# Kernel tuning notes

Measured on AMD Instinct MI355X. Metric: run time of the kernel, lower is better.

Reference implementation:

```python
import jax, jax.numpy as jnp
import numpy as np
import math

NUM_V = 32; NUM_K = 16; DK = 128; DV = 128; KCONV = 4; H = 2048
KEY_DIM = NUM_K * DK          # 2048
VALUE_DIM = NUM_V * DV        # 4096
CONV_DIM = 2 * KEY_DIM + VALUE_DIM  # 8192
EPS = 1e-6
VPK = NUM_V // NUM_K


def setup_inputs() -> dict:
    key = jax.random.key(0)
    ks = jax.random.split(key, 12)
    s = 0.02  # weight scale for numerical sanity
    return {
        "hidden_in": jax.random.normal(ks[0], (1, 1, H), jnp.float32),
        "conv_state": jax.random.normal(ks[1], (1, CONV_DIM, KCONV), jnp.float32),
        "rec_state": jax.random.normal(ks[2], (1, NUM_V, DK, DV), jnp.float32) * s,
        "W_qkv": jax.random.normal(ks[3], (CONV_DIM, H), jnp.float32) * s,
        "W_z": jax.random.normal(ks[4], (VALUE_DIM, H), jnp.float32) * s,
        "W_b": jax.random.normal(ks[5], (NUM_V, H), jnp.float32) * s,
        "W_a": jax.random.normal(ks[6], (NUM_V, H), jnp.float32) * s,
        "W_out": jax.random.normal(ks[7], (H, VALUE_DIM), jnp.float32) * s,
        "conv_w": jax.random.normal(ks[8], (CONV_DIM, KCONV), jnp.float32) * s,
        "dt_bias": jax.random.normal(ks[9], (NUM_V,), jnp.float32),
        "A_log": jax.random.normal(ks[10], (NUM_V,), jnp.float32),
        "norm_w": jnp.ones((DV,), jnp.float32),
    }


def _l2norm(x, eps=1e-6):
    return x * jax.lax.rsqrt(jnp.sum(x * x, axis=-1, keepdims=True) + eps)


def reference(hidden_in, conv_state, rec_state, W_qkv, W_z, W_b, W_a,
              W_out, conv_w, dt_bias, A_log, norm_w):
    h = hidden_in[0, 0]                       # (H,)
    mixed = W_qkv @ h                         # (CONV_DIM,)
    z = W_z @ h                               # (VALUE_DIM,)
    b = W_b @ h                               # (NUM_V,)
    a = W_a @ h                               # (NUM_V,)

    # causal conv1d update: shift state by one, take dot with kernel
    w = jnp.concatenate([conv_state, mixed[None, :, None]], axis=-1)  # (1, C, K+1)
    new_conv_state = w[:, :, 1:]                                      # (1, C, K)
    conv_out = jax.nn.silu(jnp.sum(new_conv_state * conv_w[None], axis=-1))[0]  # (C,)

    q = conv_out[:KEY_DIM].reshape(NUM_K, DK)
    k = conv_out[KEY_DIM:2 * KEY_DIM].reshape(NUM_K, DK)
    v = conv_out[2 * KEY_DIM:].reshape(NUM_V, DV)
    q = jnp.repeat(q, VPK, axis=0)            # (NUM_V, DK)
    k = jnp.repeat(k, VPK, axis=0)

    q = _l2norm(q) * (1.0 / math.sqrt(DK))
    k = _l2norm(k)

    beta = jax.nn.sigmoid(b)                                  # (NUM_V,)
    g = -jnp.exp(A_log) * jax.nn.softplus(a + dt_bias)        # (NUM_V,)

    # gated delta-rule recurrent update
    rec = rec_state[0] * jnp.exp(g)[:, None, None]            # (NUM_V, DK, DV)
    kv_mem = jnp.einsum('hkd,hk->hd', rec, k)                 # (NUM_V, DV)
    delta = (v - kv_mem) * beta[:, None]
    rec = rec + k[:, :, None] * delta[:, None, :]
    core = jnp.einsum('hkd,hk->hd', rec, q)                   # (NUM_V, DV)

    # gated RMSNorm over Dv per head
    var = jnp.mean(core * core, axis=-1, keepdims=True)
    xn = core * jax.lax.rsqrt(var + EPS) * norm_w
    zf = z.reshape(NUM_V, DV)
    out = (xn * jax.nn.silu(zf)).reshape(VALUE_DIM)

    hidden_out = (W_out @ out).reshape(1, 1, H)
    return (hidden_out, new_conv_state, rec[None])
```

## Files before the change

### kernel.cpp

```cpp
#include <hip/hip_runtime.h>

#define HDIM 2048
#define NUM_V 32
#define NUM_K 16
#define DK 128
#define DV 128
#define KEY_DIM 2048
#define VALUE_DIM 4096
#define CONV_DIM 8192
#define TOTAL_ROWS 12352



typedef __attribute__((ext_vector_type(4))) float f32x4;

__global__ __launch_bounds__(256) void k1_gemv(
    const float* __restrict__ h,
    const float* __restrict__ Wqkv,
    const float* __restrict__ Wz,
    const float* __restrict__ Wb,
    const float* __restrict__ Wa,
    const float* __restrict__ conv_state,
    const float* __restrict__ conv_w,
    float* __restrict__ ws,
    float* __restrict__ out_conv)
{
    const int row  = (blockIdx.x * 256 + threadIdx.x) >> 6;
    const int lane = threadIdx.x & 63;
    if (row >= TOTAL_ROWS) return;

    const float* wrow;
    if (row < 8192)       wrow = Wqkv + (size_t)row * HDIM;
    else if (row < 12288) wrow = Wz   + (size_t)(row - 8192) * HDIM;
    else if (row < 12320) wrow = Wb   + (size_t)(row - 12288) * HDIM;
    else                  wrow = Wa   + (size_t)(row - 12320) * HDIM;

    float acc = 0.f;
#pragma unroll
    for (int i = 0; i < 8; ++i) {
        const int idx = (i * 64 + lane) * 4;
        f32x4 w4 = *reinterpret_cast<const f32x4*>(wrow + idx);
        f32x4 h4 = *reinterpret_cast<const f32x4*>(h + idx);
        acc += w4.x * h4.x + w4.y * h4.y + w4.z * h4.z + w4.w * h4.w;
    }
#pragma unroll
    for (int off = 32; off > 0; off >>= 1)
        acc += __shfl_down(acc, off, 64);

    if (lane == 0) {
        if (row < 8192) {
            f32x4 cs = *reinterpret_cast<const f32x4*>(conv_state + row * 4);
            f32x4 cw = *reinterpret_cast<const f32x4*>(conv_w + row * 4);
            float pre = cs.y * cw.x + cs.z * cw.y + cs.w * cw.z + acc * cw.w;
            ws[row] = pre / (1.f + expf(-pre));
            f32x4 n; n.x = cs.y; n.y = cs.z; n.z = cs.w; n.w = acc;
            *reinterpret_cast<f32x4*>(out_conv + row * 4) = n;
        } else {
            ws[row] = acc;
        }
    }
}

__global__ __launch_bounds__(1024) void k2_rec(
    const float* __restrict__ ws,
    const float* __restrict__ rec_in,
    const float* __restrict__ dt_bias,
    const float* __restrict__ A_log,
    const float* __restrict__ norm_w,
    float* __restrict__ rec_out,
    float* __restrict__ out_vec)
{
    __shared__ float s_k[128];
    __shared__ float s_q[128];
    __shared__ float s_delta[128];
    __shared__ float s_part[8][128];
    __shared__ float s_red[4];

    const int hh  = blockIdx.x;
    const int t   = threadIdx.x;
    const int d   = t & 127;
    const int kkb = t >> 7;
    const int kh  = hh >> 1;

    const float bv    = ws[12288 + hh];
    const float av    = ws[12320 + hh];
    const float beta  = 1.f / (1.f + expf(-bv));
    const float x     = av + dt_bias[hh];
    const float sp    = fmaxf(x, 0.f) + log1pf(expf(-fabsf(x)));
    const float decay = expf(-expf(A_log[hh]) * sp);

    float qr = 0.f, kr = 0.f;
    if (t < 128) {
        qr = ws[kh * 128 + d];
        kr = ws[KEY_DIM + kh * 128 + d];
        float sq = qr * qr, sk = kr * kr;
#pragma unroll
        for (int off = 32; off > 0; off >>= 1) {
            sq += __shfl_down(sq, off, 64);
            sk += __shfl_down(sk, off, 64);
        }
        if ((t & 63) == 0) { s_red[t >> 6] = sq; s_red[2 + (t >> 6)] = sk; }
    }
    __syncthreads();
    if (t < 128) {
        const float ssq = s_red[0] + s_red[1];
        const float ssk = s_red[2] + s_red[3];
        s_q[d] = qr * rsqrtf(ssq + 1e-6f) * 0.08838834764831845f;
        s_k[d] = kr * rsqrtf(ssk + 1e-6f);
    }
    __syncthreads();

    const float* rrow = rec_in  + (size_t)hh * (DK * DV) + kkb * 16 * DV;
    float*       wrow = rec_out + (size_t)hh * (DK * DV) + kkb * 16 * DV;

    float rv[16];
#pragma unroll
    for (int i = 0; i < 16; ++i)
        rv[i] = rrow[i * DV + d];

    float kvp = 0.f;
#pragma unroll
    for (int i = 0; i < 16; ++i)
        kvp += rv[i] * s_k[kkb * 16 + i];
    s_part[kkb][d] = kvp;
    __syncthreads();

    if (t < 128) {
        float kv = 0.f;
#pragma unroll
        for (int j = 0; j < 8; ++j) kv += s_part[j][d];
        kv *= decay;
        const float vv = ws[2 * KEY_DIM + hh * 128 + d];
        s_delta[d] = (vv - kv) * beta;
    }
    __syncthreads();

    const float dlt = s_delta[d];
    float corep = 0.f;
#pragma unroll
    for (int i = 0; i < 16; ++i) {
        const float r = rv[i] * decay + s_k[kkb * 16 + i] * dlt;
        wrow[i * DV + d] = r;
        corep += r * s_q[kkb * 16 + i];
    }
    s_part[kkb][d] = corep;
    __syncthreads();

    float core = 0.f;
    if (t < 128) {
#pragma unroll
        for (int j = 0; j < 8; ++j) core += s_part[j][d];
        float sc = core * core;
#pragma unroll
        for (int off = 32; off > 0; off >>= 1)
            sc += __shfl_down(sc, off, 64);
        if ((t & 63) == 0) s_red[t >> 6] = sc;
    }
    __syncthreads();
    if (t < 128) {
        const float ssc = s_red[0] + s_red[1];
        const float xn  = core * rsqrtf(ssc * (1.f / 128.f) + 1e-6f) * norm_w[d];
        const float zv  = ws[8192 + hh * 128 + d];
        out_vec[hh * 128 + d] = xn * (zv / (1.f + expf(-zv)));
    }
}

__global__ __launch_bounds__(256) void k3_out(
    const float* __restrict__ Wout,
    const float* __restrict__ out_vec,
    float* __restrict__ hidden_out)
{
    const int row  = (blockIdx.x * 256 + threadIdx.x) >> 6;
    const int lane = threadIdx.x & 63;
    if (row >= HDIM) return;

    const float* wrow = Wout + (size_t)row * VALUE_DIM;
    float acc = 0.f;
#pragma unroll
    for (int i = 0; i < 16; ++i) {
        const int idx = (i * 64 + lane) * 4;
        f32x4 w4 = *reinterpret_cast<const f32x4*>(wrow + idx);
        f32x4 o4 = *reinterpret_cast<const f32x4*>(out_vec + idx);
        acc += w4.x * o4.x + w4.y * o4.y + w4.z * o4.z + w4.w * o4.w;
    }
#pragma unroll
    for (int off = 32; off > 0; off >>= 1)
        acc += __shfl_down(acc, off, 64);
    if (lane == 0) hidden_out[row] = acc;
}

extern "C" void kernel_launch(void* const* d_in, const int* in_sizes, int n_in,
                              void* d_out, int out_size, void* d_ws, size_t ws_size,
                              hipStream_t stream) {
    const float* hidden_in  = (const float*)d_in[0];
    const float* conv_state = (const float*)d_in[1];
    const float* rec_state  = (const float*)d_in[2];
    const float* W_qkv      = (const float*)d_in[3];
    const float* W_z        = (const float*)d_in[4];
    const float* W_b        = (const float*)d_in[5];
    const float* W_a        = (const float*)d_in[6];
    const float* W_out      = (const float*)d_in[7];
    const float* conv_w     = (const float*)d_in[8];
    const float* dt_bias    = (const float*)d_in[9];
    const float* A_log      = (const float*)d_in[10];
    const float* norm_w     = (const float*)d_in[11];

    float* out = (float*)d_out;
    float* ws  = (float*)d_ws;

    k1_gemv<<<TOTAL_ROWS / 4, 256, 0, stream>>>(hidden_in, W_qkv, W_z, W_b, W_a,
                                                conv_state, conv_w, ws, out + 2048);
    k2_rec<<<NUM_V, 1024, 0, stream>>>(ws, rec_state, dt_bias, A_log, norm_w,
                                       out + 2048 + CONV_DIM * 4, ws + 12352);
    k3_out<<<HDIM / 4, 256, 0, stream>>>(W_out, ws + 12352, out);
}
```

Before: 32.12 us.

## Split recurrent kernel across DV slices and move gated RMSNorm into output GEMV

Result: slower. 33.82 us (+5.3%).

```diff
diff --git a/kernel.cpp b/kernel.cpp
--- a/kernel.cpp
+++ b/kernel.cpp
@@ -9,7 +9,6 @@
 #define VALUE_DIM 4096
 #define CONV_DIM 8192
 #define TOTAL_ROWS 12352
-
 
 
 typedef __attribute__((ext_vector_type(4))) float f32x4;
@@ -66,21 +65,24 @@
     const float* __restrict__ rec_in,
     const float* __restrict__ dt_bias,
     const float* __restrict__ A_log,
-    const float* __restrict__ norm_w,
     float* __restrict__ rec_out,
-    float* __restrict__ out_vec)
+    float* __restrict__ core_out)
 {
     __shared__ float s_k[128];
     __shared__ float s_q[128];
-    __shared__ float s_delta[128];
-    __shared__ float s_part[8][128];
+    __shared__ float s_part[16][32];
+    __shared__ float s_delta[32];
     __shared__ float s_red[4];
 
-    const int hh  = blockIdx.x;
-    const int t   = threadIdx.x;
-    const int d   = t & 127;
-    const int kkb = t >> 7;
-    const int kh  = hh >> 1;
+    const int bx   = blockIdx.x;
+    const int hh   = bx >> 2;
+    const int D0   = (bx & 3) * 32;
+    const int t    = threadIdx.x;
+    const int lane = t & 63;
+    const int wid  = t >> 6;
+    const int kkb  = t >> 3;
+    const int dq4  = t & 7;
+    const int kh   = hh >> 1;
 
     const float bv    = ws[12288 + hh];
     const float av    = ws[12320 + hh];
@@ -91,8 +93,8 @@
 
     float qr = 0.f, kr = 0.f;
     if (t < 128) {
-        qr = ws[kh * 128 + d];
-        kr = ws[KEY_DIM + kh * 128 + d];
+        qr = ws[kh * 128 + t];
+        kr = ws[KEY_DIM + kh * 128 + t];
         float sq = qr * qr, sk = kr * kr;
 #pragma unroll
         for (int off = 32; off > 0; off >>= 1) {
@@ -103,84 +105,111 @@
     }
     __syncthreads();
     if (t < 128) {
-        const float ssq = s_red[0] + s_red[1];
-        const float ssk = s_red[2] + s_red[3];
-        s_q[d] = qr * rsqrtf(ssq + 1e-6f) * 0.08838834764831845f;
-        s_k[d] = kr * rsqrtf(ssk + 1e-6f);
-    }
-    __syncthreads();
-
-    const float* rrow = rec_in  + (size_t)hh * (DK * DV) + kkb * 16 * DV;
-    float*       wrow = rec_out + (size_t)hh * (DK * DV) + kkb * 16 * DV;
-
-    float rv[16];
-#pragma unroll
-    for (int i = 0; i < 16; ++i)
-        rv[i] = rrow[i * DV + d];
-
-    float kvp = 0.f;
-#pragma unroll
-    for (int i = 0; i < 16; ++i)
-        kvp += rv[i] * s_k[kkb * 16 + i];
-    s_part[kkb][d] = kvp;
-    __syncthreads();
-
-    if (t < 128) {
+        s_q[t] = qr * rsqrtf(s_red[0] + s_red[1] + 1e-6f) * 0.08838834764831845f;
+        s_k[t] = kr * rsqrtf(s_red[2] + s_red[3] + 1e-6f);
+    }
+    __syncthreads();
+
+    const size_t off0 = (size_t)hh * (DK * DV) + (size_t)kkb * DV + D0 + dq4 * 4;
+    const f32x4 rv = *reinterpret_cast<const f32x4*>(rec_in + off0);
+    const float sk = s_k[kkb];
+    const float sq = s_q[kkb];
+
+    f32x4 kvp = rv * sk;
+#pragma unroll
+    for (int off = 32; off >= 8; off >>= 1) {
+        kvp.x += __shfl_down(kvp.x, off, 64);
+        kvp.y += __shfl_down(kvp.y, off, 64);
+        kvp.z += __shfl_down(kvp.z, off, 64);
+        kvp.w += __shfl_down(kvp.w, off, 64);
+    }
+    if (lane < 8) *reinterpret_cast<f32x4*>(&s_part[wid][lane * 4]) = kvp;
+    __syncthreads();
+
+    if (t < 32) {
         float kv = 0.f;
 #pragma unroll
-        for (int j = 0; j < 8; ++j) kv += s_part[j][d];
+        for (int w = 0; w < 16; ++w) kv += s_part[w][t];
         kv *= decay;
-        const float vv = ws[2 * KEY_DIM + hh * 128 + d];
-        s_delta[d] = (vv - kv) * beta;
-    }
-    __syncthreads();
-
-    const float dlt = s_delta[d];
-    float corep = 0.f;
-#pragma unroll
-    for (int i = 0; i < 16; ++i) {
-        const float r = rv[i] * decay + s_k[kkb * 16 + i] * dlt;
-        wrow[i * DV + d] = r;
-        corep += r * s_q[kkb * 16 + i];
-    }
-    s_part[kkb][d] = corep;
-    __syncthreads();
-
-    float core = 0.f;
-    if (t < 128) {
-#pragma unroll
-        for (int j = 0; j < 8; ++j) core += s_part[j][d];
-        float sc = core * core;
-#pragma unroll
-        for (int off = 32; off > 0; off >>= 1)
-            sc += __shfl_down(sc, off, 64);
-        if ((t & 63) == 0) s_red[t >> 6] = sc;
-    }
-    __syncthreads();
-    if (t < 128) {
-        const float ssc = s_red[0] + s_red[1];
-        const float xn  = core * rsqrtf(ssc * (1.f / 128.f) + 1e-6f) * norm_w[d];
-        const float zv  = ws[8192 + hh * 128 + d];
-        out_vec[hh * 128 + d] = xn * (zv / (1.f + expf(-zv)));
+        const float vv = ws[2 * KEY_DIM + hh * 128 + D0 + t];
+        s_delta[t] = (vv - kv) * beta;
+    }
+    __syncthreads();
+
+    const f32x4 dlt = *reinterpret_cast<const f32x4*>(&s_delta[dq4 * 4]);
+    f32x4 r = rv * decay + dlt * sk;
+    *reinterpret_cast<f32x4*>(rec_out + off0) = r;
+    f32x4 cp = r * sq;
+#pragma unroll
+    for (int off = 32; off >= 8; off >>= 1) {
+        cp.x += __shfl_down(cp.x, off, 64);
+        cp.y += __shfl_down(cp.y, off, 64);
+        cp.z += __shfl_down(cp.z, off, 64);
+        cp.w += __shfl_down(cp.w, off, 64);
+    }
+    if (lane < 8) *reinterpret_cast<f32x4*>(&s_part[wid][lane * 4]) = cp;
+    __syncthreads();
+
+    if (t < 32) {
+        float core = 0.f;
+#pragma unroll
+        for (int w = 0; w < 16; ++w) core += s_part[w][t];
+        core_out[hh * 128 + D0 + t] = core;
     }
 }
 
 __global__ __launch_bounds__(256) void k3_out(
     const float* __restrict__ Wout,
-    const float* __restrict__ out_vec,
+    const float* __restrict__ ws,
+    const float* __restrict__ norm_w,
     float* __restrict__ hidden_out)
 {
-    const int row  = (blockIdx.x * 256 + threadIdx.x) >> 6;
-    const int lane = threadIdx.x & 63;
-    if (row >= HDIM) return;
-
+    __shared__ float s_ov[4096];
+    __shared__ float s_var[32];
+
+    const float* core = ws + 12352;
+    const float* z    = ws + 8192;
+    const int t    = threadIdx.x;
+    const int lane = t & 63;
+
+    {
+        float ss = 0.f;
+#pragma unroll
+        for (int q = 0; q < 4; ++q) {
+            f32x4 c4 = *reinterpret_cast<const f32x4*>(core + t * 16 + q * 4);
+            ss += c4.x * c4.x + c4.y * c4.y + c4.z * c4.z + c4.w * c4.w;
+        }
+        ss += __shfl_down(ss, 1, 64);
+        ss += __shfl_down(ss, 2, 64);
+        ss += __shfl_down(ss, 4, 64);
+        if ((t & 7) == 0) s_var[t >> 3] = ss;
+    }
+    __syncthreads();
+
+#pragma unroll
+    for (int c = 0; c < 4; ++c) {
+        const int i = (c * 256 + t) * 4;
+        f32x4 c4 = *reinterpret_cast<const f32x4*>(core + i);
+        f32x4 z4 = *reinterpret_cast<const f32x4*>(z + i);
+        f32x4 nw = *reinterpret_cast<const f32x4*>(norm_w + (i & 127));
+        const float rstd = rsqrtf(s_var[i >> 7] * (1.f / 128.f) + 1e-6f);
+        f32x4 ov;
+        ov.x = c4.x * rstd * nw.x * (z4.x / (1.f + expf(-z4.x)));
+        ov.y = c4.y * rstd * nw.y * (z4.y / (1.f + expf(-z4.y)));
+        ov.z = c4.z * rstd * nw.z * (z4.z / (1.f + expf(-z4.z)));
+        ov.w = c4.w * rstd * nw.w * (z4.w / (1.f + expf(-z4.w)));
+        *reinterpret_cast<f32x4*>(&s_ov[i]) = ov;
+    }
+    __syncthreads();
+
+    const int row = blockIdx.x * 4 + (t >> 6);
     const float* wrow = Wout + (size_t)row * VALUE_DIM;
     float acc = 0.f;
 #pragma unroll
     for (int i = 0; i < 16; ++i) {
         const int idx = (i * 64 + lane) * 4;
         f32x4 w4 = *reinterpret_cast<const f32x4*>(wrow + idx);
-        f32x4 o4 = *reinterpret_cast<const f32x4*>(out_vec + idx);
+        f32x4 o4 = *reinterpret_cast<const f32x4*>(&s_ov[idx]);
         acc += w4.x * o4.x + w4.y * o4.y + w4.z * o4.z + w4.w * o4.w;
     }
 #pragma unroll
@@ -210,7 +239,7 @@
 
     k1_gemv<<<TOTAL_ROWS / 4, 256, 0, stream>>>(hidden_in, W_qkv, W_z, W_b, W_a,
                                                 conv_state, conv_w, ws, out + 2048);
-    k2_rec<<<NUM_V, 1024, 0, stream>>>(ws, rec_state, dt_bias, A_log, norm_w,
-                                       out + 2048 + CONV_DIM * 4, ws + 12352);
-    k3_out<<<HDIM / 4, 256, 0, stream>>>(W_out, ws + 12352, out);
-}
+    k2_rec<<<NUM_V * 4, 1024, 0, stream>>>(ws, rec_state, dt_bias, A_log,
+                                           out + 2048 + CONV_DIM * 4, ws + 12352);
+    k3_out<<<HDIM / 4, 256, 0, stream>>>(W_out, ws, norm_w, out);
+}
```
